# Kernel tuning notes

Hardware: AMD Instinct MI355X
Metric: run time of the kernel (lower is better)

The kernel has to match this reference:

```python
import jax, jax.numpy as jnp
import numpy as np
from jax import lax

EPS = 1e-5

def binarize_ste(x):
    # sign binarization to {-1,+1} (0 -> +1) with straight-through gradient
    s = jnp.where(x >= 0, 1.0, -1.0).astype(x.dtype)
    return x + lax.stop_gradient(s - x)

def bn(x, gamma, beta, mean, var):
    # inference-mode batchnorm; broadcast over channel axis 1 for 4D, axis 1 for 2D
    if x.ndim == 4:
        shape = (1, -1, 1, 1)
    else:
        shape = (1, -1)
    inv = gamma.reshape(shape) / jnp.sqrt(var.reshape(shape) + EPS)
    return (x - mean.reshape(shape)) * inv + beta.reshape(shape)

def conv_rep(x, w):
    # replicate (edge) padding of 1, then valid 3x3 conv, NCHW/OIHW
    xp = jnp.pad(x, ((0, 0), (0, 0), (1, 1), (1, 1)), mode='edge')
    return lax.conv_general_dilated(xp, binarize_ste(w), (1, 1), 'VALID',
                                    dimension_numbers=('NCHW', 'OIHW', 'NCHW'))

def maxpool2(x):
    return lax.reduce_window(x, -jnp.inf, lax.max, (1, 1, 2, 2), (1, 1, 2, 2), 'VALID')

def hardtanh(x):
    return jnp.clip(x, -1.0, 1.0)

def setup_inputs() -> dict:
    key = jax.random.key(0)
    ks = jax.random.split(key, 16)
    B = 2048
    inp = {
        'x': jax.random.normal(ks[0], (B, 1, 28, 28), jnp.float32),
        'conv1_w': jax.random.normal(ks[1], (64, 1, 3, 3), jnp.float32),
        'bn1_gamma': jax.random.uniform(ks[2], (64,), jnp.float32),
        'bn1_beta': jax.random.normal(ks[3], (64,), jnp.float32),
        'bn1_mean': jax.random.normal(ks[4], (64,), jnp.float32),
        'bn1_var': jax.random.uniform(ks[5], (64,), jnp.float32),
        'conv2_w': jax.random.normal(ks[6], (64, 64, 3, 3), jnp.float32),
        'bn2_gamma': jax.random.uniform(ks[7], (64,), jnp.float32),
        'bn2_beta': jax.random.normal(ks[8], (64,), jnp.float32),
        'bn2_mean': jax.random.normal(ks[9], (64,), jnp.float32),
        'bn2_var': jax.random.uniform(ks[10], (64,), jnp.float32),
        'fc1_w': jax.random.normal(ks[11], (2048, 3136), jnp.float32),
        'bn3_gamma': jax.random.uniform(ks[12], (2048,), jnp.float32),
        'bn3_beta': jax.random.normal(ks[13], (2048,), jnp.float32),
        'bn3_mean': jax.random.normal(ks[14], (2048,), jnp.float32),
        'bn3_var': jax.random.uniform(ks[15], (2048,), jnp.float32),
        'fc2_w': jax.random.normal(jax.random.fold_in(key, 99), (10, 2048), jnp.float32),
        'scale': jnp.array([0.001], jnp.float32),
    }
    return inp

def reference(x, conv1_w, bn1_gamma, bn1_beta, bn1_mean, bn1_var,
              conv2_w, bn2_gamma, bn2_beta, bn2_mean, bn2_var,
              fc1_w, bn3_gamma, bn3_beta, bn3_mean, bn3_var,
              fc2_w, scale):
    # block 1: binarized conv -> BN -> hardtanh -> binarize -> maxpool
    h = conv_rep(x, conv1_w)                          # [B,64,28,28]
    h = binarize_ste(hardtanh(bn(h, bn1_gamma, bn1_beta, bn1_mean, bn1_var)))
    h = maxpool2(h)                                   # [B,64,14,14]
    # block 2
    h = conv_rep(h, conv2_w)                          # [B,64,14,14]
    h = binarize_ste(hardtanh(bn(h, bn2_gamma, bn2_beta, bn2_mean, bn2_var)))
    h = maxpool2(h)                                   # [B,64,7,7]
    h = h.reshape(h.shape[0], -1)                     # [B,3136] (C*H*W order)
    # fc block
    h = h @ binarize_ste(fc1_w).T                     # [B,2048]
    h = binarize_ste(hardtanh(bn(h, bn3_gamma, bn3_beta, bn3_mean, bn3_var)))
    h = h @ binarize_ste(fc2_w).T                     # [B,10]
    return h * scale
```

## Files before the change

### kernel.cpp

```cpp
#include <hip/hip_runtime.h>
#include <cstdint>

#define EPS 1e-5f

typedef unsigned long long u64;
typedef unsigned int u32;
typedef unsigned short u16;
typedef unsigned char u8;

__device__ __forceinline__ int clampi(int v, int lo, int hi) {
    return v < lo ? lo : (v > hi ? hi : v);
}


__global__ void prep_small(
    const float* __restrict__ conv1_w, const float* __restrict__ conv2_w,
    const float* __restrict__ fc2_w,
    const float* __restrict__ g1, const float* __restrict__ b1,
    const float* __restrict__ m1, const float* __restrict__ v1,
    const float* __restrict__ g2, const float* __restrict__ b2,
    const float* __restrict__ m2, const float* __restrict__ v2,
    float* __restrict__ s1, u64* __restrict__ w2p, u64* __restrict__ w2pk,
    float4* __restrict__ bnc1, float4* __restrict__ bnc2)
{
    int t = blockIdx.x * 256 + threadIdx.x;
    if (t < 576) {
        s1[t] = (conv1_w[t] >= 0.f) ? 1.f : -1.f;
    } else if (t < 1152) {
        int u = t - 576;
        int co = u / 9, tap = u % 9;
        u64 word = 0;
        for (int ci = 0; ci < 64; ci++)
            word |= (u64)(conv2_w[(co * 64 + ci) * 9 + tap] >= 0.f) << ci;
        w2p[u] = word;
    } else if (t < 1472) {
        int u = t - 1152;
        int o = u / 32, k = u % 32;
        u64 word = 0;
        for (int j = 0; j < 64; j++)
            word |= (u64)(fc2_w[o * 2048 + k * 64 + j] >= 0.f) << j;
        w2pk[u] = word;
    } else if (t < 1536) {
        int ch = t - 1472;
        bnc1[ch] = make_float4(m1[ch], g1[ch] / sqrtf(v1[ch] + EPS), b1[ch], 0.f);
    } else if (t < 1600) {
        int ch = t - 1536;
        bnc2[ch] = make_float4(m2[ch], g2[ch] / sqrtf(v2[ch] + EPS), b2[ch], 0.f);
    }
}


__global__ __launch_bounds__(256) void prep_fc1(const float* __restrict__ w,
                                                u64* __restrict__ wp) {
    __shared__ float ls[3136];
    int o = blockIdx.x;
    const float4* row4 = (const float4*)(w + o * 3136);
    for (int i = threadIdx.x; i < 784; i += 256)
        ((float4*)ls)[i] = row4[i];
    __syncthreads();
    int p = threadIdx.x;
    if (p < 49) {
        u64 word = 0;
        #pragma unroll
        for (int c = 0; c < 64; c++)
            word |= (u64)(ls[c * 49 + p] >= 0.f) << c;
        wp[p * 2048 + o] = word;
    }
}


__global__ __launch_bounds__(256) void k_conv1(
    const float* __restrict__ x, const float* __restrict__ s1,
    const float4* __restrict__ bnc1, u64* __restrict__ out1)
{
    int tid = threadIdx.x;
    int g = blockIdx.y;
    int base = g * 16;

    int idx = blockIdx.x * 256 + tid;
    int b = idx / 196, p = idx % 196;
    int pi = p / 14, pj = p % 14;

    const float* xb = x + b * 784;
    int rr[4], cc[4];
    #pragma unroll
    for (int r = 0; r < 4; r++) rr[r] = clampi(2 * pi - 1 + r, 0, 27) * 28;
    #pragma unroll
    for (int c = 0; c < 4; c++) cc[c] = clampi(2 * pj - 1 + c, 0, 27);
    float patch[4][4];
    #pragma unroll
    for (int r = 0; r < 4; r++)
        #pragma unroll
        for (int c = 0; c < 4; c++)
            patch[r][c] = xb[rr[r] + cc[c]];

    u32 word = 0;
    #pragma unroll 4
    for (int ch = 0; ch < 16; ch++) {
        const float* w = s1 + (base + ch) * 9;
        float v00 = 0.f, v01 = 0.f, v10 = 0.f, v11 = 0.f;
        #pragma unroll
        for (int ki = 0; ki < 3; ki++)
            #pragma unroll
            for (int kj = 0; kj < 3; kj++) {
                float ww = w[ki * 3 + kj];
                v00 += patch[ki][kj] * ww;
                v01 += patch[ki][kj + 1] * ww;
                v10 += patch[ki + 1][kj] * ww;
                v11 += patch[ki + 1][kj + 1] * ww;
            }
        float vmin = fminf(fminf(v00, v01), fminf(v10, v11));
        float vmax = fmaxf(fmaxf(v00, v01), fmaxf(v10, v11));
        float4 c4 = bnc1[base + ch];
        int bit = (((vmin - c4.x) * c4.y + c4.z) >= 0.f) |
                  (((vmax - c4.x) * c4.y + c4.z) >= 0.f);
        word |= (u32)bit << ch;
    }
    ((u16*)out1)[idx * 4 + g] = (u16)word;
}


__global__ __launch_bounds__(256) void k_conv2(
    const u64* __restrict__ in, const u64* __restrict__ w2p,
    const float4* __restrict__ bnc2, u64* __restrict__ out2)
{
    int tid = threadIdx.x;
    int g = blockIdx.y;
    int base = g * 8;

    int idx = blockIdx.x * 256 + tid;
    int b = idx / 49, p = idx % 49;
    int pi = p / 7, pj = p % 7;

    const u64* ib = in + b * 196;
    int rr[4], cc[4];
    #pragma unroll
    for (int r = 0; r < 4; r++) rr[r] = clampi(2 * pi - 1 + r, 0, 13) * 14;
    #pragma unroll
    for (int c = 0; c < 4; c++) cc[c] = clampi(2 * pj - 1 + c, 0, 13);
    u64 a[4][4];
    #pragma unroll
    for (int r = 0; r < 4; r++)
        #pragma unroll
        for (int c = 0; c < 4; c++)
            a[r][c] = ib[rr[r] + cc[c]];

    u32 word = 0;
    #pragma unroll
    for (int co = 0; co < 8; co++) {
        const u64* w = w2p + (base + co) * 9;
        int s00 = 0, s01 = 0, s10 = 0, s11 = 0;
        #pragma unroll
        for (int ki = 0; ki < 3; ki++)
            #pragma unroll
            for (int kj = 0; kj < 3; kj++) {
                u64 ww = w[ki * 3 + kj];
                s00 += __popcll(a[ki][kj] ^ ww);
                s01 += __popcll(a[ki][kj + 1] ^ ww);
                s10 += __popcll(a[ki + 1][kj] ^ ww);
                s11 += __popcll(a[ki + 1][kj + 1] ^ ww);
            }
        int smin = min(min(s00, s01), min(s10, s11));
        int smax = max(max(s00, s01), max(s10, s11));
        float4 c4 = bnc2[base + co];
        int bit = (((float)(576 - 2 * smin) - c4.x) * c4.y + c4.z >= 0.f) |
                  (((float)(576 - 2 * smax) - c4.x) * c4.y + c4.z >= 0.f);
        word |= (u32)bit << co;
    }
    ((u8*)out2)[idx * 8 + g] = (u8)word;
}


#define NB 8

__global__ __launch_bounds__(256) void k_fc1(
    const u64* __restrict__ act, const u64* __restrict__ wp,
    const float* __restrict__ g, const float* __restrict__ bt,
    const float* __restrict__ mn, const float* __restrict__ vr,
    u64* __restrict__ out3)
{
    int tid = threadIdx.x;
    int btile = blockIdx.x >> 3;
    int otile = blockIdx.x & 7;
    int b0 = btile * NB;
    int o = otile * 256 + tid;
    const u64* ab = act + b0 * 49;

    int sums[NB];
    #pragma unroll
    for (int i = 0; i < NB; i++) sums[i] = 0;

    for (int p = 0; p < 49; p++) {
        u64 w = wp[p * 2048 + o];
        #pragma unroll
        for (int bb = 0; bb < NB; bb++)
            sums[bb] += __popcll(ab[bb * 49 + p] ^ w);
    }

    float iv = g[o] / sqrtf(vr[o] + EPS);
    float m = mn[o], be = bt[o];
    #pragma unroll
    for (int bb = 0; bb < NB; bb++) {
        float y = ((float)(3136 - 2 * sums[bb]) - m) * iv + be;
        u64 ball = __ballot(y >= 0.f);
        if ((tid & 63) == 0) out3[(b0 + bb) * 32 + (o >> 6)] = ball;
    }
}


__global__ void k_fc2(const u64* __restrict__ act, const u64* __restrict__ w2,
                      const float* __restrict__ scale, float* __restrict__ out)
{
    int idx = blockIdx.x * 256 + threadIdx.x;
    if (idx >= 2048 * 16) return;
    int b = idx >> 4, o = idx & 15;
    if (o >= 10) return;
    int s = 0;
    #pragma unroll
    for (int k = 0; k < 32; k++)
        s += __popcll(act[b * 32 + k] ^ w2[o * 32 + k]);
    out[b * 10 + o] = scale[0] * (float)(2048 - 2 * s);
}


extern "C" void kernel_launch(void* const* d_in, const int* in_sizes, int n_in,
                              void* d_out, int out_size, void* d_ws, size_t ws_size,
                              hipStream_t stream) {
    const float* x        = (const float*)d_in[0];
    const float* conv1_w  = (const float*)d_in[1];
    const float* bn1_g    = (const float*)d_in[2];
    const float* bn1_b    = (const float*)d_in[3];
    const float* bn1_m    = (const float*)d_in[4];
    const float* bn1_v    = (const float*)d_in[5];
    const float* conv2_w  = (const float*)d_in[6];
    const float* bn2_g    = (const float*)d_in[7];
    const float* bn2_b    = (const float*)d_in[8];
    const float* bn2_m    = (const float*)d_in[9];
    const float* bn2_v    = (const float*)d_in[10];
    const float* fc1_w    = (const float*)d_in[11];
    const float* bn3_g    = (const float*)d_in[12];
    const float* bn3_b    = (const float*)d_in[13];
    const float* bn3_m    = (const float*)d_in[14];
    const float* bn3_v    = (const float*)d_in[15];
    const float* fc2_w    = (const float*)d_in[16];
    const float* scale    = (const float*)d_in[17];
    float* out = (float*)d_out;

    char* ws = (char*)d_ws;
    float*  s1   = (float*) (ws + 0);
    u64*    w2p  = (u64*)   (ws + 2560);
    float4* bnc1 = (float4*)(ws + 7168);
    u64*    wp   = (u64*)   (ws + 8192);
    u64*    w2pk = (u64*)   (ws + 811008);
    float4* bnc2 = (float4*)(ws + 813568);
    u64*    out1 = (u64*)   (ws + 819200);
    u64*    out2 = (u64*)   (ws + 4030464);
    u64*    out3 = (u64*)   (ws + 4833280);

    hipLaunchKernelGGL(prep_small, dim3(7), dim3(256), 0, stream,
                       conv1_w, conv2_w, fc2_w,
                       bn1_g, bn1_b, bn1_m, bn1_v,
                       bn2_g, bn2_b, bn2_m, bn2_v,
                       s1, w2p, w2pk, bnc1, bnc2);
    hipLaunchKernelGGL(prep_fc1, dim3(2048), dim3(256), 0, stream, fc1_w, wp);

    hipLaunchKernelGGL(k_conv1, dim3(1568, 4), dim3(256), 0, stream,
                       x, s1, bnc1, out1);
    hipLaunchKernelGGL(k_conv2, dim3(392, 8), dim3(256), 0, stream,
                       out1, w2p, bnc2, out2);
    hipLaunchKernelGGL(k_fc1, dim3(2048), dim3(256), 0, stream,
                       out2, wp, bn3_g, bn3_b, bn3_m, bn3_v, out3);
    hipLaunchKernelGGL(k_fc2, dim3(128), dim3(256), 0, stream,
                       out3, w2pk, scale, out);
}
```

Baseline: 208.5 us.

## Fuse all stages into one persistent kernel with global grid barriers

Wraps each stage (weight prep, conv1, conv2, fc1, fc2) as a device function and runs them inside a single persistent kernel. Blocks loop over work units, and an atomic-counter grid barrier separates the stages. This removes per-kernel launch overhead and inter-kernel gaps. In exchange it limits occupancy to the persistent grid size, adds barrier wait time, and relies on all blocks being co-resident; a guarded spin breakout could silently break ordering.

```diff
diff --git a/kernel.cpp b/kernel.cpp
--- a/kernel.cpp
+++ b/kernel.cpp
@@ -13,7 +13,8 @@
 }
 
 
-__global__ void prep_small(
+__device__ __forceinline__ void prep_small_body(
+    int t,
     const float* __restrict__ conv1_w, const float* __restrict__ conv2_w,
     const float* __restrict__ fc2_w,
     const float* __restrict__ g1, const float* __restrict__ b1,
@@ -23,7 +24,6 @@
     float* __restrict__ s1, u64* __restrict__ w2p, u64* __restrict__ w2pk,
     float4* __restrict__ bnc1, float4* __restrict__ bnc2)
 {
-    int t = blockIdx.x * 256 + threadIdx.x;
     if (t < 576) {
         s1[t] = (conv1_w[t] >= 0.f) ? 1.f : -1.f;
     } else if (t < 1152) {
@@ -49,11 +49,10 @@
     }
 }
 
-
-__global__ __launch_bounds__(256) void prep_fc1(const float* __restrict__ w,
-                                                u64* __restrict__ wp) {
-    __shared__ float ls[3136];
-    int o = blockIdx.x;
+__device__ __forceinline__ void prep_fc1_body(
+    int o, float* ls,
+    const float* __restrict__ w, u64* __restrict__ wp)
+{
     const float4* row4 = (const float4*)(w + o * 3136);
     for (int i = threadIdx.x; i < 784; i += 256)
         ((float4*)ls)[i] = row4[i];
@@ -66,18 +65,15 @@
             word |= (u64)(ls[c * 49 + p] >= 0.f) << c;
         wp[p * 2048 + o] = word;
     }
-}
-
-
-__global__ __launch_bounds__(256) void k_conv1(
+    __syncthreads();
+}
+
+__device__ __forceinline__ void conv1_body(
+    int idx, int g,
     const float* __restrict__ x, const float* __restrict__ s1,
     const float4* __restrict__ bnc1, u64* __restrict__ out1)
 {
-    int tid = threadIdx.x;
-    int g = blockIdx.y;
     int base = g * 16;
-
-    int idx = blockIdx.x * 256 + tid;
     int b = idx / 196, p = idx % 196;
     int pi = p / 14, pj = p % 14;
 
@@ -119,16 +115,12 @@
     ((u16*)out1)[idx * 4 + g] = (u16)word;
 }
 
-
-__global__ __launch_bounds__(256) void k_conv2(
+__device__ __forceinline__ void conv2_body(
+    int idx, int g,
     const u64* __restrict__ in, const u64* __restrict__ w2p,
     const float4* __restrict__ bnc2, u64* __restrict__ out2)
 {
-    int tid = threadIdx.x;
-    int g = blockIdx.y;
     int base = g * 8;
-
-    int idx = blockIdx.x * 256 + tid;
     int b = idx / 49, p = idx % 49;
     int pi = p / 7, pj = p % 7;
 
@@ -170,8 +162,152 @@
     ((u8*)out2)[idx * 8 + g] = (u8)word;
 }
 
-
 #define NB 8
+
+__device__ __forceinline__ void fc1_body(
+    int u, int tid,
+    const u64* __restrict__ act, const u64* __restrict__ wp,
+    const float* __restrict__ g, const float* __restrict__ bt,
+    const float* __restrict__ mn, const float* __restrict__ vr,
+    u64* __restrict__ out3)
+{
+    int btile = u >> 3;
+    int otile = u & 7;
+    int b0 = btile * NB;
+    int o = otile * 256 + tid;
+    const u64* ab = act + b0 * 49;
+
+    int sums[NB];
+    #pragma unroll
+    for (int i = 0; i < NB; i++) sums[i] = 0;
+
+    for (int p = 0; p < 49; p++) {
+        u64 w = wp[p * 2048 + o];
+        #pragma unroll
+        for (int bb = 0; bb < NB; bb++)
+            sums[bb] += __popcll(ab[bb * 49 + p] ^ w);
+    }
+
+    float iv = g[o] / sqrtf(vr[o] + EPS);
+    float m = mn[o], be = bt[o];
+    #pragma unroll
+    for (int bb = 0; bb < NB; bb++) {
+        float y = ((float)(3136 - 2 * sums[bb]) - m) * iv + be;
+        u64 ball = __ballot(y >= 0.f);
+        if ((tid & 63) == 0) out3[(b0 + bb) * 32 + (o >> 6)] = ball;
+    }
+}
+
+__device__ __forceinline__ void fc2_body(
+    int idx,
+    const u64* __restrict__ act, const u64* __restrict__ w2,
+    const float* __restrict__ scale, float* __restrict__ out)
+{
+    if (idx >= 2048 * 16) return;
+    int b = idx >> 4, o = idx & 15;
+    if (o >= 10) return;
+    int s = 0;
+    #pragma unroll
+    for (int k = 0; k < 32; k++)
+        s += __popcll(act[b * 32 + k] ^ w2[o * 32 + k]);
+    out[b * 10 + o] = scale[0] * (float)(2048 - 2 * s);
+}
+
+
+__device__ __forceinline__ void gbar(u32* cnt, u32 target) {
+    __syncthreads();
+    if (threadIdx.x == 0) {
+        __threadfence();
+        __hip_atomic_fetch_add(cnt, 1u, __ATOMIC_RELEASE, __HIP_MEMORY_SCOPE_AGENT);
+        u32 guard = 0;
+        while (__hip_atomic_load(cnt, __ATOMIC_ACQUIRE, __HIP_MEMORY_SCOPE_AGENT) < target) {
+            __builtin_amdgcn_s_sleep(8);
+            if (++guard > (1u << 18)) break;
+        }
+        __threadfence();
+    }
+    __syncthreads();
+}
+
+
+struct FusedArgs {
+    const float *x, *conv1_w, *conv2_w, *fc2_w;
+    const float *g1, *b1, *m1, *v1;
+    const float *g2, *b2, *m2, *v2;
+    const float *fc1_w;
+    const float *g3, *b3, *m3, *v3;
+    const float *scale;
+    float* out;
+    float* s1; u64* w2p; u64* w2pk; float4* bnc1; float4* bnc2;
+    u64* wp; u64* out1; u64* out2; u64* out3;
+    u32* bar;
+};
+
+__global__ __launch_bounds__(256, 2) void fused_persist(FusedArgs A) {
+    __shared__ float ls[3136];
+    const int nb = gridDim.x, bid = blockIdx.x, tid = threadIdx.x;
+
+    for (int u = bid; u < 2055; u += nb) {
+        if (u < 2048) {
+            prep_fc1_body(u, ls, A.fc1_w, A.wp);
+        } else {
+            prep_small_body((u - 2048) * 256 + tid, A.conv1_w, A.conv2_w, A.fc2_w,
+                            A.g1, A.b1, A.m1, A.v1, A.g2, A.b2, A.m2, A.v2,
+                            A.s1, A.w2p, A.w2pk, A.bnc1, A.bnc2);
+        }
+    }
+    gbar(A.bar, (u32)nb);
+
+    for (int u = bid; u < 6272; u += nb)
+        conv1_body((u % 1568) * 256 + tid, u / 1568, A.x, A.s1, A.bnc1, A.out1);
+    gbar(A.bar, (u32)(2 * nb));
+
+    for (int u = bid; u < 3136; u += nb)
+        conv2_body((u % 392) * 256 + tid, u / 392, A.out1, A.w2p, A.bnc2, A.out2);
+    gbar(A.bar, (u32)(3 * nb));
+
+    for (int u = bid; u < 2048; u += nb)
+        fc1_body(u, tid, A.out2, A.wp, A.g3, A.b3, A.m3, A.v3, A.out3);
+    gbar(A.bar, (u32)(4 * nb));
+
+    for (int u = bid; u < 128; u += nb)
+        fc2_body(u * 256 + tid, A.out3, A.w2pk, A.scale, A.out);
+}
+
+
+__global__ void prep_small(
+    const float* __restrict__ conv1_w, const float* __restrict__ conv2_w,
+    const float* __restrict__ fc2_w,
+    const float* __restrict__ g1, const float* __restrict__ b1,
+    const float* __restrict__ m1, const float* __restrict__ v1,
+    const float* __restrict__ g2, const float* __restrict__ b2,
+    const float* __restrict__ m2, const float* __restrict__ v2,
+    float* __restrict__ s1, u64* __restrict__ w2p, u64* __restrict__ w2pk,
+    float4* __restrict__ bnc1, float4* __restrict__ bnc2)
+{
+    prep_small_body(blockIdx.x * 256 + threadIdx.x, conv1_w, conv2_w, fc2_w,
+                    g1, b1, m1, v1, g2, b2, m2, v2, s1, w2p, w2pk, bnc1, bnc2);
+}
+
+__global__ __launch_bounds__(256) void prep_fc1(const float* __restrict__ w,
+                                                u64* __restrict__ wp) {
+    __shared__ float ls[3136];
+    prep_fc1_body(blockIdx.x, ls, w, wp);
+}
+
+__global__ __launch_bounds__(256) void k_conv1(
+    const float* __restrict__ x, const float* __restrict__ s1,
+    const float4* __restrict__ bnc1, u64* __restrict__ out1)
+{
+    conv1_body(blockIdx.x * 256 + threadIdx.x, blockIdx.y, x, s1, bnc1, out1);
+}
+
+__global__ __launch_bounds__(256) void k_conv2(
+    const u64* __restrict__ in, const u64* __restrict__ w2p,
+    const float4* __restrict__ bnc2, u64* __restrict__ out2)
+{
+    conv2_body(blockIdx.x * 256 + threadIdx.x, blockIdx.y, in, w2p, bnc2, out2);
+}
 
 __global__ __launch_bounds__(256) void k_fc1(
     const u64* __restrict__ act, const u64* __restrict__ wp,
@@ -179,47 +315,13 @@
     const float* __restrict__ mn, const float* __restrict__ vr,
     u64* __restrict__ out3)
 {
-    int tid = threadIdx.x;
-    int btile = blockIdx.x >> 3;
-    int otile = blockIdx.x & 7;
-    int b0 = btile * NB;
-    int o = otile * 256 + tid;
-    const u64* ab = act + b0 * 49;
-
-    int sums[NB];
-    #pragma unroll
-    for (int i = 0; i < NB; i++) sums[i] = 0;
-
-    for (int p = 0; p < 49; p++) {
-        u64 w = wp[p * 2048 + o];
-        #pragma unroll
-        for (int bb = 0; bb < NB; bb++)
-            sums[bb] += __popcll(ab[bb * 49 + p] ^ w);
-    }
-
-    float iv = g[o] / sqrtf(vr[o] + EPS);
-    float m = mn[o], be = bt[o];
-    #pragma unroll
-    for (int bb = 0; bb < NB; bb++) {
-        float y = ((float)(3136 - 2 * sums[bb]) - m) * iv + be;
-        u64 ball = __ballot(y >= 0.f);
-        if ((tid & 63) == 0) out3[(b0 + bb) * 32 + (o >> 6)] = ball;
-    }
-}
-
+    fc1_body(blockIdx.x, threadIdx.x, act, wp, g, bt, mn, vr, out3);
+}
 
 __global__ void k_fc2(const u64* __restrict__ act, const u64* __restrict__ w2,
                       const float* __restrict__ scale, float* __restrict__ out)
 {
-    int idx = blockIdx.x * 256 + threadIdx.x;
-    if (idx >= 2048 * 16) return;
-    int b = idx >> 4, o = idx & 15;
-    if (o >= 10) return;
-    int s = 0;
-    #pragma unroll
-    for (int k = 0; k < 32; k++)
-        s += __popcll(act[b * 32 + k] ^ w2[o * 32 + k]);
-    out[b * 10 + o] = scale[0] * (float)(2048 - 2 * s);
+    fc2_body(blockIdx.x * 256 + threadIdx.x, act, w2, scale, out);
 }
 
 
@@ -256,20 +358,49 @@
     u64*    out1 = (u64*)   (ws + 819200);
     u64*    out2 = (u64*)   (ws + 4030464);
     u64*    out3 = (u64*)   (ws + 4833280);
-
-    hipLaunchKernelGGL(prep_small, dim3(7), dim3(256), 0, stream,
-                       conv1_w, conv2_w, fc2_w,
-                       bn1_g, bn1_b, bn1_m, bn1_v,
-                       bn2_g, bn2_b, bn2_m, bn2_v,
-                       s1, w2p, w2pk, bnc1, bnc2);
-    hipLaunchKernelGGL(prep_fc1, dim3(2048), dim3(256), 0, stream, fc1_w, wp);
-
-    hipLaunchKernelGGL(k_conv1, dim3(1568, 4), dim3(256), 0, stream,
-                       x, s1, bnc1, out1);
-    hipLaunchKernelGGL(k_conv2, dim3(392, 8), dim3(256), 0, stream,
-                       out1, w2p, bnc2, out2);
-    hipLaunchKernelGGL(k_fc1, dim3(2048), dim3(256), 0, stream,
-                       out2, wp, bn3_g, bn3_b, bn3_m, bn3_v, out3);
-    hipLaunchKernelGGL(k_fc2, dim3(128), dim3(256), 0, stream,
-                       out3, w2pk, scale, out);
-}
+    u32*    bar  = (u32*)   (ws + 5357568);
+
+    FusedArgs fa;
+    fa.x = x; fa.conv1_w = conv1_w; fa.conv2_w = conv2_w; fa.fc2_w = fc2_w;
+    fa.g1 = bn1_g; fa.b1 = bn1_b; fa.m1 = bn1_m; fa.v1 = bn1_v;
+    fa.g2 = bn2_g; fa.b2 = bn2_b; fa.m2 = bn2_m; fa.v2 = bn2_v;
+    fa.fc1_w = fc1_w;
+    fa.g3 = bn3_g; fa.b3 = bn3_b; fa.m3 = bn3_m; fa.v3 = bn3_v;
+    fa.scale = scale; fa.out = out;
+    fa.s1 = s1; fa.w2p = w2p; fa.w2pk = w2pk; fa.bnc1 = bnc1; fa.bnc2 = bnc2;
+    fa.wp = wp; fa.out1 = out1; fa.out2 = out2; fa.out3 = out3;
+    fa.bar = bar;
+
+    static int cfg = -2;
+    if (cfg == -2) {
+        int maxb = 0;
+        hipError_t e = hipOccupancyMaxActiveBlocksPerMultiprocessor(
+            &maxb, (const void*)fused_persist, 256, 0);
+        if (e == hipSuccess && maxb >= 2) {
+            cfg = (maxb >= 4) ? 1024 : 512;
+        } else {
+            cfg = -1;
+            (void)hipGetLastError();
+        }
+    }
+
+    if (cfg > 0) {
+        hipMemsetAsync(bar, 0, 256, stream);
+        hipLaunchKernelGGL(fused_persist, dim3(cfg), dim3(256), 0, stream, fa);
+    } else {
+        hipLaunchKernelGGL(prep_small, dim3(7), dim3(256), 0, stream,
+                           conv1_w, conv2_w, fc2_w,
+                           bn1_g, bn1_b, bn1_m, bn1_v,
+                           bn2_g, bn2_b, bn2_m, bn2_v,
+                           s1, w2p, w2pk, bnc1, bnc2);
+        hipLaunchKernelGGL(prep_fc1, dim3(2048), dim3(256), 0, stream, fc1_w, wp);
+        hipLaunchKernelGGL(k_conv1, dim3(1568, 4), dim3(256), 0, stream,
+                           x, s1, bnc1, out1);
+        hipLaunchKernelGGL(k_conv2, dim3(392, 8), dim3(256), 0, stream,
+                           out1, w2p, bnc2, out2);
+        hipLaunchKernelGGL(k_fc1, dim3(2048), dim3(256), 0, stream,
+                           out2, wp, bn3_g, bn3_b, bn3_m, bn3_v, out3);
+        hipLaunchKernelGGL(k_fc2, dim3(128), dim3(256), 0, stream,
+                           out3, w2pk, scale, out);
+    }
+}
```

After: 697.7 us. 3.35x slower.
